# Performance work log

Measured on AMD Instinct MI355X. Metric: run time of the kernel, lower is better.

## Reference

```python
import jax, jax.numpy as jnp
import numpy as np

NEG_SLOPE = 0.01  # torch nn.LeakyReLU default


def setup_inputs() -> dict:
    key = jax.random.key(0)
    k1, k2, k3, k4 = jax.random.split(key, 4)
    N, D_IN, D_OUT = 8192, 200, 128
    H = jax.random.normal(k1, (N, D_IN), dtype=jnp.float32)
    A = jax.random.normal(k2, (N, N), dtype=jnp.float32)
    W = jax.random.normal(k3, (D_IN, D_OUT), dtype=jnp.float32) * (1.0 / np.sqrt(D_IN))
    b = jax.random.normal(k4, (D_OUT,), dtype=jnp.float32) * 0.01
    return {"H": H, "A": A, "W": W, "b": b}


def reference(H, A, W, b):
    # A = clamp(sigmoid(A), min=0.1)
    A = jnp.maximum(jax.nn.sigmoid(A), 0.1)
    # D^-1/2 A D^-1/2 -- diag matmuls are equivalent to row/col broadcast scaling
    d_inv_sqrt = jnp.power(A.sum(axis=1), -0.5)  # [N]
    A_hat = A * d_inv_sqrt[:, None] * d_inv_sqrt[None, :]
    # Linear then aggregate
    HW = H @ W + b  # [N, D_OUT]
    out = A_hat @ HW
    out = jnp.where(out >= 0, out, NEG_SLOPE * out)  # LeakyReLU
    return out, A
```

## Files before the change

kernel.cpp:

```cpp
#include <hip/hip_runtime.h>
#include <hip/hip_bf16.h>

#define NR 8192
#define DIN 200
#define DOUT 128

#define NSPLIT 4
#define KSPL 2048
#define BK 32
#define LDK 40
#define NIT 64

typedef __attribute__((ext_vector_type(8))) short short8;
typedef __attribute__((ext_vector_type(4))) float f32x4;
typedef __attribute__((ext_vector_type(4))) float fv4;
typedef __attribute__((ext_vector_type(4))) unsigned short u16x4;

__device__ __forceinline__ unsigned short f2bf(float x) {
    union { float f; unsigned u; } v; v.f = x;
    unsigned r = v.u + 0x7FFFu + ((v.u >> 16) & 1u);
    return (unsigned short)(r >> 16);
}

__device__ __forceinline__ fv4 sig4(fv4 x) {
    fv4 s;
    s[0] = fmaxf(__builtin_amdgcn_rcpf(1.f + __expf(-x[0])), 0.1f);
    s[1] = fmaxf(__builtin_amdgcn_rcpf(1.f + __expf(-x[1])), 0.1f);
    s[2] = fmaxf(__builtin_amdgcn_rcpf(1.f + __expf(-x[2])), 0.1f);
    s[3] = fmaxf(__builtin_amdgcn_rcpf(1.f + __expf(-x[3])), 0.1f);
    return s;
}

__global__ __launch_bounds__(256) void k_sum(const float* __restrict__ A,
                                             float* __restrict__ A2,
                                             unsigned short* __restrict__ SA,
                                             float* __restrict__ dis) {
    const int row = blockIdx.x;
    const fv4* __restrict__ ar = (const fv4*)(A + (size_t)row * NR);
    fv4* __restrict__ a2r = (fv4*)(A2 + (size_t)row * NR);
    u16x4* __restrict__ sar = (u16x4*)(SA + (size_t)row * NR);
    float sum = 0.f;
#pragma unroll
    for (int i = 0; i < 8; ++i) {
        const int idx = i * 256 + threadIdx.x;
        fv4 x = __builtin_nontemporal_load(&ar[idx]);
        fv4 s = sig4(x);
        __builtin_nontemporal_store(s, &a2r[idx]);
        u16x4 pk;
        pk[0] = f2bf(s[0]); pk[1] = f2bf(s[1]); pk[2] = f2bf(s[2]); pk[3] = f2bf(s[3]);
        sar[idx] = pk;
        sum += (s[0] + s[1]) + (s[2] + s[3]);
    }
#pragma unroll
    for (int off = 32; off > 0; off >>= 1) sum += __shfl_down(sum, off, 64);
    __shared__ float red[4];
    if ((threadIdx.x & 63) == 0) red[threadIdx.x >> 6] = sum;
    __syncthreads();
    if (threadIdx.x == 0)
        dis[row] = __builtin_amdgcn_rsqf((red[0] + red[1]) + (red[2] + red[3]));
}

__global__ __launch_bounds__(256) void k_vt(const float* __restrict__ H,
                                            const float* __restrict__ W,
                                            const float* __restrict__ bias,
                                            const float* __restrict__ dis,
                                            unsigned short* __restrict__ VT) {
    __shared__ float hs[32 * 201];
    const int rowBase = blockIdx.x * 32;
    for (int i = threadIdx.x; i < 32 * DIN; i += 256) {
        int r = i / DIN;
        int k = i - r * DIN;
        hs[r * 201 + k] = H[(size_t)rowBase * DIN + i];
    }
    __syncthreads();
    const int c0 = (threadIdx.x & 31) * 4;
    const int rg = threadIdx.x >> 5;
    float acc[4][4];
#pragma unroll
    for (int r = 0; r < 4; ++r)
#pragma unroll
        for (int i = 0; i < 4; ++i) acc[r][i] = 0.f;
#pragma unroll 4
    for (int k = 0; k < DIN; ++k) {
        float4 w4 = *(const float4*)(W + k * DOUT + c0);
#pragma unroll
        for (int r = 0; r < 4; ++r) {
            float h = hs[(rg * 4 + r) * 201 + k];
            acc[r][0] = fmaf(h, w4.x, acc[r][0]);
            acc[r][1] = fmaf(h, w4.y, acc[r][1]);
            acc[r][2] = fmaf(h, w4.z, acc[r][2]);
            acc[r][3] = fmaf(h, w4.w, acc[r][3]);
        }
    }
    float4 b4 = *(const float4*)(bias + c0);
    float bb[4] = {b4.x, b4.y, b4.z, b4.w};
    float dsc[4];
#pragma unroll
    for (int r = 0; r < 4; ++r) dsc[r] = dis[rowBase + rg * 4 + r];
#pragma unroll
    for (int i = 0; i < 4; ++i) {
        ushort4 pk;
        pk.x = f2bf(dsc[0] * (acc[0][i] + bb[i]));
        pk.y = f2bf(dsc[1] * (acc[1][i] + bb[i]));
        pk.z = f2bf(dsc[2] * (acc[2][i] + bb[i]));
        pk.w = f2bf(dsc[3] * (acc[3][i] + bb[i]));
        *(ushort4*)(VT + (size_t)(c0 + i) * NR + rowBase + rg * 4) = pk;
    }
}

__global__ __launch_bounds__(256, 4) void k_gemm(const unsigned short* __restrict__ SA,
                                                 const unsigned short* __restrict__ VT,
                                                 float* __restrict__ P) {
    __shared__ alignas(16) unsigned short lA[2][32 * LDK];
    __shared__ alignas(16) unsigned short lV[2][128 * LDK];
    const int tid = threadIdx.x;
    const int blockRow = blockIdx.x & 255;
    const int s = blockIdx.x >> 8;
    const int rowBase = blockRow * 32;
    const size_t kb0 = (size_t)s * KSPL;

    const int am = tid >> 3, ak = (tid & 7) * 4;
    const unsigned short* __restrict__ ap = SA + (size_t)(rowBase + am) * NR + kb0 + ak;
    const int vc = tid >> 2, vq = (tid & 3) * 8;
    const unsigned short* __restrict__ vp0 = VT + (size_t)vc * NR + kb0 + vq;
    const unsigned short* __restrict__ vp1 = vp0 + (size_t)64 * NR;

    const int lane = tid & 63, w = tid >> 6;
    const int rt = w & 1, cg = w >> 1;
    const int fm = lane & 15, kq = lane >> 4;

    f32x4 acc[4];
#pragma unroll
    for (int nt = 0; nt < 4; ++nt) {
        acc[nt][0] = 0.f; acc[nt][1] = 0.f; acc[nt][2] = 0.f; acc[nt][3] = 0.f;
    }

    u16x4 ga; short8 gv0, gv1;

    ga  = *(const u16x4*)(ap);
    gv0 = *(const short8*)(vp0);
    gv1 = *(const short8*)(vp1);
    *(u16x4*)(&lA[0][am * LDK + ak]) = ga;
    *(short8*)(&lV[0][vc * LDK + vq]) = gv0;
    *(short8*)(&lV[0][(vc + 64) * LDK + vq]) = gv1;
    ga  = *(const u16x4*)(ap + BK);
    gv0 = *(const short8*)(vp0 + BK);
    gv1 = *(const short8*)(vp1 + BK);

    const unsigned short* lap = &lA[0][(rt * 16 + fm) * LDK + kq * 8];
    const unsigned short* lvp = &lV[0][(cg * 64 + fm) * LDK + kq * 8];
    const int strideA = 32 * LDK;
    const int strideV = 128 * LDK;

    for (int i = 0; i < NIT; ++i) {
        __syncthreads();
        if (i + 1 < NIT) {
            const int nb = (i + 1) & 1;
            *(u16x4*)(&lA[nb][am * LDK + ak]) = ga;
            *(short8*)(&lV[nb][vc * LDK + vq]) = gv0;
            *(short8*)(&lV[nb][(vc + 64) * LDK + vq]) = gv1;
        }
        if (i + 2 < NIT) {
            const size_t off = (size_t)(i + 2) * BK;
            ga  = *(const u16x4*)(ap + off);
            gv0 = *(const short8*)(vp0 + off);
            gv1 = *(const short8*)(vp1 + off);
        }
        const int cb = i & 1;
        short8 a8 = *(const short8*)(lap + cb * strideA);
#pragma unroll
        for (int nt = 0; nt < 4; ++nt) {
            short8 b8 = *(const short8*)(lvp + cb * strideV + nt * 16 * LDK);
            acc[nt] = __builtin_amdgcn_mfma_f32_16x16x32_bf16(a8, b8, acc[nt], 0, 0, 0);
        }
    }

    float* __restrict__ Pp = P + (size_t)s * ((size_t)NR * DOUT);
    const int row0 = rowBase + rt * 16 + kq * 4;
    const int col0 = cg * 64 + fm;
#pragma unroll
    for (int nt = 0; nt < 4; ++nt) {
#pragma unroll
        for (int v = 0; v < 4; ++v) {
            Pp[(size_t)(row0 + v) * DOUT + col0 + nt * 16] = acc[nt][v];
        }
    }
}

__global__ __launch_bounds__(256) void k_comb(const float* __restrict__ P,
                                              const float* __restrict__ dis,
                                              float* __restrict__ out) {
    const int idx = blockIdx.x * 256 + threadIdx.x;
    const float d = dis[idx >> 5];
    const size_t sl = (size_t)NR * DOUT;
    const fv4 p0 = *(const fv4*)(P + (size_t)idx * 4);
    const fv4 p1 = *(const fv4*)(P + (size_t)idx * 4 + sl);
    const fv4 p2 = *(const fv4*)(P + (size_t)idx * 4 + 2 * sl);
    const fv4 p3 = *(const fv4*)(P + (size_t)idx * 4 + 3 * sl);
    fv4 t = (p0 + p1) + (p2 + p3);
    fv4 o;
#pragma unroll
    for (int j = 0; j < 4; ++j) {
        float v = d * t[j];
        o[j] = v >= 0.f ? v : 0.01f * v;
    }
    *(fv4*)(out + (size_t)idx * 4) = o;
}

extern "C" void kernel_launch(void* const* d_in, const int* in_sizes, int n_in,
                              void* d_out, int out_size, void* d_ws, size_t ws_size,
                              hipStream_t stream) {
    const float* H = (const float*)d_in[0];
    const float* A = (const float*)d_in[1];
    const float* W = (const float*)d_in[2];
    const float* b = (const float*)d_in[3];

    float* out = (float*)d_out;
    float* A2  = out + (size_t)NR * DOUT;

    char* ws = (char*)d_ws;
    float* dis = (float*)ws;
    unsigned short* VT = (unsigned short*)(ws + 65536);
    float* P = (float*)(ws + (4ull << 20));
    unsigned short* SA = (unsigned short*)(ws + (20ull << 20));

    k_sum <<<NR,   256, 0, stream>>>(A, A2, SA, dis);
    k_vt  <<<256,  256, 0, stream>>>(H, W, b, dis, VT);
    k_gemm<<<1024, 256, 0, stream>>>(SA, VT, P);
    k_comb<<<1024, 256, 0, stream>>>(P, dis, out);
}
```

Before: 527.3 us.

## Double split-K in aggregation GEMM and retile waves as 2x2 MFMA blocks

The split-K factor of the A_hat·V GEMM goes from 4 to 8, launching twice as many blocks with half the K range each. Each wave now computes a 2x2 grid of 16x16 MFMA tiles instead of a 1x4 strip, so A and V fragments loaded from LDS are each reused twice. The occupancy hint rises to 6 blocks per CU. The combine kernel loops over all eight partials and uses nontemporal loads and stores. The cost is doubled partial-sum traffic through the P buffer, for which the workspace is re-laid out.

```diff
diff --git a/kernel.cpp b/kernel.cpp
--- a/kernel.cpp
+++ b/kernel.cpp
@@ -5,11 +5,11 @@
 #define DIN 200
 #define DOUT 128
 
-#define NSPLIT 4
-#define KSPL 2048
+#define NSPLIT 8
+#define KSPL 1024
 #define BK 32
 #define LDK 40
-#define NIT 64
+#define NIT 32
 
 typedef __attribute__((ext_vector_type(8))) short short8;
 typedef __attribute__((ext_vector_type(4))) float f32x4;
@@ -108,7 +108,7 @@
     }
 }
 
-__global__ __launch_bounds__(256, 4) void k_gemm(const unsigned short* __restrict__ SA,
+__global__ __launch_bounds__(256, 6) void k_gemm(const unsigned short* __restrict__ SA,
                                                  const unsigned short* __restrict__ VT,
                                                  float* __restrict__ P) {
     __shared__ alignas(16) unsigned short lA[2][32 * LDK];
@@ -126,14 +126,16 @@
     const unsigned short* __restrict__ vp1 = vp0 + (size_t)64 * NR;
 
     const int lane = tid & 63, w = tid >> 6;
-    const int rt = w & 1, cg = w >> 1;
     const int fm = lane & 15, kq = lane >> 4;
 
-    f32x4 acc[4];
-#pragma unroll
-    for (int nt = 0; nt < 4; ++nt) {
-        acc[nt][0] = 0.f; acc[nt][1] = 0.f; acc[nt][2] = 0.f; acc[nt][3] = 0.f;
-    }
+    f32x4 acc[2][2];
+#pragma unroll
+    for (int m = 0; m < 2; ++m)
+#pragma unroll
+        for (int nt = 0; nt < 2; ++nt) {
+            acc[m][nt][0] = 0.f; acc[m][nt][1] = 0.f;
+            acc[m][nt][2] = 0.f; acc[m][nt][3] = 0.f;
+        }
 
     u16x4 ga; short8 gv0, gv1;
 
@@ -147,8 +149,8 @@
     gv0 = *(const short8*)(vp0 + BK);
     gv1 = *(const short8*)(vp1 + BK);
 
-    const unsigned short* lap = &lA[0][(rt * 16 + fm) * LDK + kq * 8];
-    const unsigned short* lvp = &lV[0][(cg * 64 + fm) * LDK + kq * 8];
+    const unsigned short* lap = &lA[0][fm * LDK + kq * 8];
+    const unsigned short* lvp = &lV[0][(w * 32 + fm) * LDK + kq * 8];
     const int strideA = 32 * LDK;
     const int strideV = 128 * LDK;
 
@@ -167,22 +169,27 @@
             gv1 = *(const short8*)(vp1 + off);
         }
         const int cb = i & 1;
-        short8 a8 = *(const short8*)(lap + cb * strideA);
-#pragma unroll
-        for (int nt = 0; nt < 4; ++nt) {
-            short8 b8 = *(const short8*)(lvp + cb * strideV + nt * 16 * LDK);
-            acc[nt] = __builtin_amdgcn_mfma_f32_16x16x32_bf16(a8, b8, acc[nt], 0, 0, 0);
-        }
+        short8 a0 = *(const short8*)(lap + cb * strideA);
+        short8 a1 = *(const short8*)(lap + cb * strideA + 16 * LDK);
+        short8 b0 = *(const short8*)(lvp + cb * strideV);
+        short8 b1 = *(const short8*)(lvp + cb * strideV + 16 * LDK);
+        acc[0][0] = __builtin_amdgcn_mfma_f32_16x16x32_bf16(a0, b0, acc[0][0], 0, 0, 0);
+        acc[0][1] = __builtin_amdgcn_mfma_f32_16x16x32_bf16(a0, b1, acc[0][1], 0, 0, 0);
+        acc[1][0] = __builtin_amdgcn_mfma_f32_16x16x32_bf16(a1, b0, acc[1][0], 0, 0, 0);
+        acc[1][1] = __builtin_amdgcn_mfma_f32_16x16x32_bf16(a1, b1, acc[1][1], 0, 0, 0);
     }
 
     float* __restrict__ Pp = P + (size_t)s * ((size_t)NR * DOUT);
-    const int row0 = rowBase + rt * 16 + kq * 4;
-    const int col0 = cg * 64 + fm;
-#pragma unroll
-    for (int nt = 0; nt < 4; ++nt) {
-#pragma unroll
-        for (int v = 0; v < 4; ++v) {
-            Pp[(size_t)(row0 + v) * DOUT + col0 + nt * 16] = acc[nt][v];
+#pragma unroll
+    for (int m = 0; m < 2; ++m) {
+        const int row0 = rowBase + m * 16 + kq * 4;
+#pragma unroll
+        for (int nt = 0; nt < 2; ++nt) {
+            const int col0 = w * 32 + nt * 16 + fm;
+#pragma unroll
+            for (int v = 0; v < 4; ++v) {
+                Pp[(size_t)(row0 + v) * DOUT + col0] = acc[m][nt][v];
+            }
         }
     }
 }
@@ -193,18 +200,19 @@
     const int idx = blockIdx.x * 256 + threadIdx.x;
     const float d = dis[idx >> 5];
     const size_t sl = (size_t)NR * DOUT;
-    const fv4 p0 = *(const fv4*)(P + (size_t)idx * 4);
-    const fv4 p1 = *(const fv4*)(P + (size_t)idx * 4 + sl);
-    const fv4 p2 = *(const fv4*)(P + (size_t)idx * 4 + 2 * sl);
-    const fv4 p3 = *(const fv4*)(P + (size_t)idx * 4 + 3 * sl);
-    fv4 t = (p0 + p1) + (p2 + p3);
+    fv4 t = {0.f, 0.f, 0.f, 0.f};
+#pragma unroll
+    for (int sp = 0; sp < NSPLIT; ++sp) {
+        fv4 p = __builtin_nontemporal_load((const fv4*)(P + (size_t)idx * 4 + sp * sl));
+        t += p;
+    }
     fv4 o;
 #pragma unroll
     for (int j = 0; j < 4; ++j) {
         float v = d * t[j];
         o[j] = v >= 0.f ? v : 0.01f * v;
     }
-    *(fv4*)(out + (size_t)idx * 4) = o;
+    __builtin_nontemporal_store(o, (fv4*)(out + (size_t)idx * 4));
 }
 
 extern "C" void kernel_launch(void* const* d_in, const int* in_sizes, int n_in,
@@ -222,10 +230,10 @@
     float* dis = (float*)ws;
     unsigned short* VT = (unsigned short*)(ws + 65536);
     float* P = (float*)(ws + (4ull << 20));
-    unsigned short* SA = (unsigned short*)(ws + (20ull << 20));
+    unsigned short* SA = (unsigned short*)(ws + (40ull << 20));
 
     k_sum <<<NR,   256, 0, stream>>>(A, A2, SA, dis);
     k_vt  <<<256,  256, 0, stream>>>(H, W, b, dis, VT);
-    k_gemm<<<1024, 256, 0, stream>>>(SA, VT, P);
+    k_gemm<<<2048, 256, 0, stream>>>(SA, VT, P);
     k_comb<<<1024, 256, 0, stream>>>(P, dis, out);
 }
```

Measured after the change: 527.5 us. About the same (+0.0%).
